# Kernel optimization log

Measured on AMD Instinct MI355X. Metric: run time of the kernel, lower is better.

The kernel has to match this reference:

```python
import jax, jax.numpy as jnp
import numpy as np

N = 50000
E = 800000
DIM_IN, DIM_H, DIM_OUT, HEADS = 128, 8, 32, 15
NEG_SLOPE = 0.2  # PyG GATv2Conv default


def gatv2_layer(x, src, dst, Wl, Wr, att, bias, num_nodes):
    """PyG GATv2Conv (share_weights=False, concat=True) with self-loops already in src/dst.
    x: [N, F_in]; Wl/Wr: [F_in, H*C]; att: [H, C]; bias: [H*C].
    """
    H, C = att.shape
    xl = (x @ Wl).reshape(-1, H, C)  # source transform [N,H,C]
    xr = (x @ Wr).reshape(-1, H, C)  # target transform [N,H,C]
    s = jax.nn.leaky_relu(xl[src] + xr[dst], negative_slope=NEG_SLOPE)  # [E,H,C]
    e = jnp.einsum('ehc,hc->eh', s, att)  # attention logits [E,H]
    # numerically-stable segment softmax over incoming edges of each dst node
    emax = jax.ops.segment_max(e, dst, num_segments=num_nodes)  # [N,H]
    ee = jnp.exp(e - emax[dst])
    denom = jax.ops.segment_sum(ee, dst, num_segments=num_nodes)  # [N,H]
    alpha = ee / denom[dst]  # self-loops guarantee denom > 0
    out = jax.ops.segment_sum(alpha[:, :, None] * xl[src], dst, num_segments=num_nodes)  # [N,H,C]
    return out.reshape(num_nodes, H * C) + bias


def setup_inputs() -> dict:
    key = jax.random.key(0)
    ks = jax.random.split(key, 10)
    x = jax.random.normal(ks[0], (N, DIM_IN), dtype=jnp.float32)
    edge_index = jax.random.randint(ks[1], (2, E), 0, N, dtype=jnp.int64)
    g1 = 1.0 / np.sqrt(DIM_IN)
    g2 = 1.0 / np.sqrt(DIM_H * HEADS)
    return {
        'x': x,
        'edge_index': edge_index,
        'W1l': jax.random.normal(ks[2], (DIM_IN, HEADS * DIM_H), dtype=jnp.float32) * g1,
        'W1r': jax.random.normal(ks[3], (DIM_IN, HEADS * DIM_H), dtype=jnp.float32) * g1,
        'att1': jax.random.normal(ks[4], (HEADS, DIM_H), dtype=jnp.float32) * (1.0 / np.sqrt(DIM_H)),
        'b1': jnp.zeros((HEADS * DIM_H,), dtype=jnp.float32),
        'W2l': jax.random.normal(ks[5], (HEADS * DIM_H, DIM_OUT), dtype=jnp.float32) * g2,
        'W2r': jax.random.normal(ks[6], (HEADS * DIM_H, DIM_OUT), dtype=jnp.float32) * g2,
        'att2': jax.random.normal(ks[7], (1, DIM_OUT), dtype=jnp.float32) * (1.0 / np.sqrt(DIM_OUT)),
        'b2': jnp.zeros((DIM_OUT,), dtype=jnp.float32),
    }


def reference(x, edge_index, W1l, W1r, att1, b1, W2l, W2r, att2, b2):
    n = x.shape[0]
    loops = jnp.arange(n, dtype=edge_index.dtype)
    src = jnp.concatenate([edge_index[0], loops])  # PyG add_self_loops=True
    dst = jnp.concatenate([edge_index[1], loops])
    h = gatv2_layer(x, src, dst, W1l, W1r, att1, b1, n)  # [N, HEADS*DIM_H]
    h = jax.nn.elu(h)
    # dropout(p=0.3) is identity in eval mode
    h = gatv2_layer(h, src, dst, W2l, W2r, att2, b2, n)  # heads=1 -> [N, DIM_OUT]
    return h, jax.nn.log_softmax(h, axis=1)
```

## Files before the change

kernel.cpp:

```cpp
#include <hip/hip_runtime.h>
#include <math.h>

namespace {
constexpr int NN  = 50000;
constexpr int EE  = 800000;
constexpr int FIN = 128;
constexpr int HC1 = 120;
constexpr int F2  = 32;
constexpr int MT  = NN / 16;
constexpr int CAP = 64;
constexpr int NBIN = 64;
constexpr int BINW = 782;
constexpr int BINCAP = 16384;
constexpr int TILE = 4096;
constexpr int ABLK = (EE + TILE - 1) / TILE;
constexpr int CHUNKW = 12500;
}

typedef __attribute__((ext_vector_type(8))) short bf16x8;
typedef __attribute__((ext_vector_type(4))) float f32x4;

template<int CTRL>
__device__ __forceinline__ float dppf(float x) {
    return __int_as_float(__builtin_amdgcn_mov_dpp(__float_as_int(x), CTRL, 0xF, 0xF, true));
}
__device__ __forceinline__ float quad_sum(float x) {
    x += dppf<0xB1>(x);
    x += dppf<0x4E>(x);
    return x;
}
template<int MASK>
__device__ __forceinline__ float swz_add(float x) {
    return x + __int_as_float(__builtin_amdgcn_ds_swizzle(__float_as_int(x), (MASK << 10) | 0x1F));
}
template<int MASK>
__device__ __forceinline__ float swz_max(float x) {
    return fmaxf(x, __int_as_float(__builtin_amdgcn_ds_swizzle(__float_as_int(x), (MASK << 10) | 0x1F)));
}

__device__ __forceinline__ unsigned short f2bf(float f) {
    unsigned int u = __float_as_uint(f);
    unsigned int r = (u + 0x7fffu + ((u >> 16) & 1u)) >> 16;
    return (unsigned short)r;
}
__device__ __forceinline__ float2 bf2f2(unsigned int u) {
    return make_float2(__uint_as_float(u << 16), __uint_as_float(u & 0xffff0000u));
}

__global__ void prep_init_kernel(const unsigned int* __restrict__ raw,
                                 const float* __restrict__ W1l, const float* __restrict__ W1r,
                                 const float* __restrict__ W2l, const float* __restrict__ W2r,
                                 unsigned short* __restrict__ Bf1, unsigned short* __restrict__ Bf2,
                                 int* __restrict__ cursor, int* __restrict__ flag) {
    int tid = blockIdx.x * blockDim.x + threadIdx.x;
    if (blockIdx.x == 0 && threadIdx.x < 64) {
        int t = threadIdx.x;
        unsigned int hi = raw[2 * t + 1];
        unsigned long long ball = __ballot(hi == 0u);
        if (t == 0) *flag = (ball == ~0ULL) ? 1 : 0;
    }
    if (tid < 4096) {
        int t = tid >> 8, lane = tid & 63;
        int kb = (tid >> 6) & 3;
        int k0 = kb * 32 + (lane >> 4) * 8;
        int n = (t & 7) * 16 + (lane & 15);
        const float* W = (t < 8) ? W1l : W1r;
        #pragma unroll
        for (int j = 0; j < 8; ++j)
            Bf1[(size_t)tid * 8 + j] = (n < HC1) ? f2bf(W[(k0 + j) * HC1 + n]) : (unsigned short)0;
    } else if (tid < 5120) {
        int id = tid - 4096;
        int t = id >> 8, lane = id & 63;
        int kb = (id >> 6) & 3;
        int k0 = kb * 32 + (lane >> 4) * 8;
        int nl = (t & 1) * 16 + (lane & 15);
        const float* W = (t < 2) ? W2l : W2r;
        #pragma unroll
        for (int j = 0; j < 8; ++j) {
            int k = k0 + j;
            Bf2[(size_t)id * 8 + j] = (k < HC1) ? f2bf(W[k * F2 + nl]) : (unsigned short)0;
        }
    } else if (tid >= 8192 && tid < 8192 + NBIN) {
        cursor[tid - 8192] = 0;
    }
}

__global__ void __launch_bounds__(256) binA_kernel(
    const unsigned int* __restrict__ raw, const int* __restrict__ flag,
    int* __restrict__ cursor, unsigned int* __restrict__ binbuf) {
    __shared__ int lcnt[NBIN];
    __shared__ int lbase[NBIN];
    __shared__ int lcnt2[NBIN];
    int tid = threadIdx.x;
    int e0 = blockIdx.x * TILE;
    int is64 = *flag;
    if (tid < NBIN) { lcnt[tid] = 0; lcnt2[tid] = 0; }
    __syncthreads();
    #pragma unroll
    for (int i = 0; i < TILE / 256; ++i) {
        int e = e0 + i * 256 + tid;
        if (e < EE) {
            int d = is64 ? (int)raw[2 * (size_t)(EE + e)] : (int)raw[EE + e];
            atomicAdd(&lcnt[d / BINW], 1);
        }
    }
    __syncthreads();
    if (tid < NBIN) {
        int c = lcnt[tid];
        lbase[tid] = (c > 0) ? atomicAdd(&cursor[tid], c) : 0;
    }
    __syncthreads();
    #pragma unroll
    for (int i = 0; i < TILE / 256; ++i) {
        int e = e0 + i * 256 + tid;
        if (e < EE) {
            unsigned int s = is64 ? raw[2 * (size_t)e] : raw[e];
            unsigned int d = is64 ? raw[2 * (size_t)(EE + e)] : raw[EE + e];
            int bin = (int)d / BINW;
            int pos = lbase[bin] + atomicAdd(&lcnt2[bin], 1);
            if (pos < BINCAP) binbuf[(size_t)bin * BINCAP + pos] = (s << 16) | d;
        }
    }
}

__global__ void __launch_bounds__(1024) binB_kernel(
    const int* __restrict__ cursor, const unsigned int* __restrict__ binbuf,
    int* __restrict__ cnt, unsigned short* __restrict__ bucket) {
    __shared__ int lc[BINW * 4];
    int g = blockIdx.x;
    int tid = threadIdx.x;
    int ng0 = g * BINW;
    for (int i = tid; i < BINW * 4; i += 1024) lc[i] = 0;
    __syncthreads();
    int m = min(cursor[g], BINCAP);
    const unsigned int* bb = binbuf + (size_t)g * BINCAP;
    for (int i = tid; i < m; i += 1024) {
        unsigned int u = bb[i];
        int d = (int)(u & 0xffffu);
        int s = (int)(u >> 16);
        atomicAdd(&lc[(d - ng0) * 4 + s / CHUNKW], 1);
    }
    __syncthreads();
    if (tid < BINW) {
        int c0 = lc[tid * 4], c1 = lc[tid * 4 + 1], c2 = lc[tid * 4 + 2], c3 = lc[tid * 4 + 3];
        lc[tid * 4] = 0;
        lc[tid * 4 + 1] = c0;
        lc[tid * 4 + 2] = c0 + c1;
        lc[tid * 4 + 3] = c0 + c1 + c2;
        int n = ng0 + tid;
        if (n < NN) cnt[n] = min(c0 + c1 + c2 + c3, CAP);
    }
    __syncthreads();
    for (int i = tid; i < m; i += 1024) {
        unsigned int u = bb[i];
        int d = (int)(u & 0xffffu);
        int s = (int)(u >> 16);
        int pos = atomicAdd(&lc[(d - ng0) * 4 + s / CHUNKW], 1);
        if (pos < CAP) bucket[(size_t)d * CAP + pos] = (unsigned short)s;
    }
}

__global__ void __launch_bounds__(256) gemm1_mfma_kernel(
    const float* __restrict__ x, const unsigned short* __restrict__ Bf,
    unsigned short* __restrict__ xlb, unsigned short* __restrict__ xrb) {
    int wave = threadIdx.x >> 6, lane = threadIdx.x & 63;
    int mt = blockIdx.x * 4 + wave;
    if (mt >= MT) return;
    int n0 = mt * 16;
    int lr = lane & 15, kg = lane >> 4;
    const float* xrow = x + (size_t)(n0 + lr) * FIN + kg * 8;
    bf16x8 a[4];
    #pragma unroll
    for (int ko = 0; ko < 4; ++ko) {
        float4 lo = *(const float4*)(xrow + ko * 32);
        float4 hi = *(const float4*)(xrow + ko * 32 + 4);
        union { unsigned int u[4]; bf16x8 v; } cv;
        cv.u[0] = f2bf(lo.x) | ((unsigned int)f2bf(lo.y) << 16);
        cv.u[1] = f2bf(lo.z) | ((unsigned int)f2bf(lo.w) << 16);
        cv.u[2] = f2bf(hi.x) | ((unsigned int)f2bf(hi.y) << 16);
        cv.u[3] = f2bf(hi.z) | ((unsigned int)f2bf(hi.w) << 16);
        a[ko] = cv.v;
    }
    const bf16x8* bp = (const bf16x8*)Bf + lane;
    f32x4 acc[16];
    #pragma unroll
    for (int t = 0; t < 16; ++t) acc[t] = (f32x4){0.f, 0.f, 0.f, 0.f};
    #pragma unroll
    for (int t = 0; t < 16; ++t) {
        bf16x8 b0 = bp[(t * 4 + 0) * 64];
        bf16x8 b1 = bp[(t * 4 + 1) * 64];
        bf16x8 b2 = bp[(t * 4 + 2) * 64];
        bf16x8 b3 = bp[(t * 4 + 3) * 64];
        acc[t] = __builtin_amdgcn_mfma_f32_16x16x32_bf16(a[0], b0, acc[t], 0, 0, 0);
        acc[t] = __builtin_amdgcn_mfma_f32_16x16x32_bf16(a[1], b1, acc[t], 0, 0, 0);
        acc[t] = __builtin_amdgcn_mfma_f32_16x16x32_bf16(a[2], b2, acc[t], 0, 0, 0);
        acc[t] = __builtin_amdgcn_mfma_f32_16x16x32_bf16(a[3], b3, acc[t], 0, 0, 0);
    }
    #pragma unroll
    for (int t = 0; t < 16; ++t) {
        unsigned short* outp = (t < 8) ? xlb : xrb;
        int cg = (t & 7) * 16 + lr;
        if (cg < HC1) {
            #pragma unroll
            for (int r = 0; r < 4; ++r)
                outp[(size_t)(n0 + kg * 4 + r) * HC1 + cg] = f2bf(acc[t][r]);
        }
    }
}

__global__ void __launch_bounds__(256) fused1_kernel(
    const unsigned short* __restrict__ bucket, const int* __restrict__ cnt,
    const unsigned short* __restrict__ xlb, const unsigned short* __restrict__ xrb,
    const float* __restrict__ att, const float* __restrict__ b1,
    unsigned int* __restrict__ hout) {
    __shared__ int s_src[4][64];
    int wave = threadIdx.x >> 6;
    int lane = threadIdx.x & 63;
    int n = blockIdx.x * 4 + wave;
    bool act = lane < 60;
    int c0 = act ? 2 * lane : 0;
    float2 xrv = bf2f2(*(const unsigned int*)(xrb + (size_t)n * HC1 + c0));
    float2 atv = *(const float2*)(att + c0);
    int deg = min(cnt[n], CAP);
    int srcv = (lane < deg) ? (int)bucket[(size_t)n * CAP + lane] : 0;
    s_src[wave][lane] = srcv;
    float s, o0, o1;
    {
        unsigned int ua = *(const unsigned int*)(xlb + (size_t)n * HC1 + c0);
        float2 ra = bf2f2(ua);
        float t0 = ra.x + xrv.x; t0 = fmaxf(t0, 0.2f * t0);
        float t1 = ra.y + xrv.y; t1 = fmaxf(t1, 0.2f * t1);
        float pa = quad_sum(atv.x * t0 + atv.y * t1);
        float ea = __expf(fminf(pa, 60.f));
        s = ea; o0 = ea * ra.x; o1 = ea * ra.y;
    }
    for (int j = 0; j < deg; j += 2) {
        int2 ss = *(const int2*)&s_src[wave][j];
        unsigned int ua = *(const unsigned int*)(xlb + (size_t)ss.x * HC1 + c0);
        unsigned int ub = *(const unsigned int*)(xlb + (size_t)ss.y * HC1 + c0);
        float2 ra = bf2f2(ua);
        float2 rb = bf2f2(ub);
        float t0, t1;
        t0 = ra.x + xrv.x; t0 = fmaxf(t0, 0.2f * t0);
        t1 = ra.y + xrv.y; t1 = fmaxf(t1, 0.2f * t1);
        float pa = atv.x * t0 + atv.y * t1;
        t0 = rb.x + xrv.x; t0 = fmaxf(t0, 0.2f * t0);
        t1 = rb.y + xrv.y; t1 = fmaxf(t1, 0.2f * t1);
        float pb = atv.x * t0 + atv.y * t1;
        pa = quad_sum(pa);
        pb = quad_sum(pb);
        float ea = __expf(fminf(pa, 60.f));
        float eb = (j + 1 < deg) ? __expf(fminf(pb, 60.f)) : 0.f;
        s += ea + eb;
        o0 = fmaf(eb, rb.x, fmaf(ea, ra.x, o0));
        o1 = fmaf(eb, rb.y, fmaf(ea, ra.y, o1));
    }
    unsigned int packed = 0u;
    if (act) {
        float inv = 1.0f / s;
        float2 bv = *(const float2*)(b1 + c0);
        float v0 = o0 * inv + bv.x;
        float v1 = o1 * inv + bv.y;
        v0 = v0 > 0.f ? v0 : __expf(v0) - 1.f;
        v1 = v1 > 0.f ? v1 : __expf(v1) - 1.f;
        packed = (unsigned int)f2bf(v0) | ((unsigned int)f2bf(v1) << 16);
    }
    hout[(size_t)n * 64 + lane] = packed;
}

__global__ void __launch_bounds__(256) gemm2_mfma_kernel(
    const unsigned short* __restrict__ hb, const unsigned short* __restrict__ Bf,
    unsigned short* __restrict__ xl2b, unsigned short* __restrict__ xr2b) {
    int wave = threadIdx.x >> 6, lane = threadIdx.x & 63;
    int mt = blockIdx.x * 4 + wave;
    if (mt >= MT) return;
    int n0 = mt * 16;
    int lr = lane & 15, kg = lane >> 4;
    const unsigned short* ab = hb + (size_t)(n0 + lr) * FIN + kg * 8;
    bf16x8 a0 = *(const bf16x8*)(ab);
    bf16x8 a1 = *(const bf16x8*)(ab + 32);
    bf16x8 a2 = *(const bf16x8*)(ab + 64);
    bf16x8 a3 = *(const bf16x8*)(ab + 96);
    const bf16x8* bp = (const bf16x8*)Bf + lane;
    f32x4 acc[4];
    #pragma unroll
    for (int t = 0; t < 4; ++t) acc[t] = (f32x4){0.f, 0.f, 0.f, 0.f};
    #pragma unroll
    for (int t = 0; t < 4; ++t) {
        bf16x8 b0 = bp[(t * 4 + 0) * 64];
        bf16x8 b1 = bp[(t * 4 + 1) * 64];
        bf16x8 b2 = bp[(t * 4 + 2) * 64];
        bf16x8 b3 = bp[(t * 4 + 3) * 64];
        acc[t] = __builtin_amdgcn_mfma_f32_16x16x32_bf16(a0, b0, acc[t], 0, 0, 0);
        acc[t] = __builtin_amdgcn_mfma_f32_16x16x32_bf16(a1, b1, acc[t], 0, 0, 0);
        acc[t] = __builtin_amdgcn_mfma_f32_16x16x32_bf16(a2, b2, acc[t], 0, 0, 0);
        acc[t] = __builtin_amdgcn_mfma_f32_16x16x32_bf16(a3, b3, acc[t], 0, 0, 0);
    }
    #pragma unroll
    for (int t = 0; t < 4; ++t) {
        unsigned short* outp = (t < 2) ? xl2b : xr2b;
        int cg = (t & 1) * 16 + lr;
        #pragma unroll
        for (int r = 0; r < 4; ++r)
            outp[(size_t)(n0 + kg * 4 + r) * F2 + cg] = f2bf(acc[t][r]);
    }
}

__global__ void __launch_bounds__(256) fused2_kernel(
    const unsigned short* __restrict__ bucket, const int* __restrict__ cnt,
    const unsigned short* __restrict__ xl2b, const unsigned short* __restrict__ xr2b,
    const float* __restrict__ att2, const float* __restrict__ b2,
    float* __restrict__ out) {
    __shared__ int s_src[4][64];
    int wave = threadIdx.x >> 6;
    int lane = threadIdx.x & 63;
    int n = blockIdx.x * 4 + wave;
    int grp = lane >> 4;
    int cl = lane & 15;
    int c0 = 2 * cl;
    float2 xrv = bf2f2(*(const unsigned int*)(xr2b + (size_t)n * F2 + c0));
    float2 atv = *(const float2*)(att2 + c0);
    int deg = min(cnt[n], CAP);
    int srcv = (lane < deg) ? (int)bucket[(size_t)n * CAP + lane] : 0;
    s_src[wave][lane] = srcv;
    float s, o0, o1;
    {
        unsigned int u = *(const unsigned int*)(xl2b + (size_t)n * F2 + c0);
        float2 r = bf2f2(u);
        float t0 = r.x + xrv.x; t0 = fmaxf(t0, 0.2f * t0);
        float t1 = r.y + xrv.y; t1 = fmaxf(t1, 0.2f * t1);
        float p = atv.x * t0 + atv.y * t1;
        p = quad_sum(p);
        p = swz_add<4>(p);
        p = swz_add<8>(p);
        float e = (grp == 0) ? __expf(fminf(p, 60.f)) : 0.f;
        s = e; o0 = e * r.x; o1 = e * r.y;
    }
    for (int j = 0; j < deg; j += 4) {
        int myj = j + grp;
        int src = s_src[wave][min(myj, 63)];
        bool val = myj < deg;
        unsigned int u = *(const unsigned int*)(xl2b + (size_t)src * F2 + c0);
        float2 r = bf2f2(u);
        float t0 = r.x + xrv.x; t0 = fmaxf(t0, 0.2f * t0);
        float t1 = r.y + xrv.y; t1 = fmaxf(t1, 0.2f * t1);
        float p = atv.x * t0 + atv.y * t1;
        p = quad_sum(p);
        p = swz_add<4>(p);
        p = swz_add<8>(p);
        float e = val ? __expf(fminf(p, 60.f)) : 0.f;
        s += e;
        o0 = fmaf(e, r.x, o0);
        o1 = fmaf(e, r.y, o1);
    }
    s  = swz_add<16>(s);   s  += __shfl_xor(s, 32);
    o0 = swz_add<16>(o0);  o0 += __shfl_xor(o0, 32);
    o1 = swz_add<16>(o1);  o1 += __shfl_xor(o1, 32);
    float2 bv = *(const float2*)(b2 + c0);
    float inv = 1.0f / s;
    float v0 = o0 * inv + bv.x;
    float v1 = o1 * inv + bv.y;
    float mm = fmaxf(v0, v1);
    mm = fmaxf(mm, dppf<0xB1>(mm));
    mm = fmaxf(mm, dppf<0x4E>(mm));
    mm = swz_max<4>(mm);
    mm = swz_max<8>(mm);
    float se = __expf(v0 - mm) + __expf(v1 - mm);
    se += dppf<0xB1>(se);
    se += dppf<0x4E>(se);
    se = swz_add<4>(se);
    se = swz_add<8>(se);
    float lse = mm + __logf(se);
    if (lane < 16) {
        *(float2*)(out + (size_t)n * F2 + c0) = make_float2(v0, v1);
        *(float2*)(out + (size_t)NN * F2 + (size_t)n * F2 + c0) =
            make_float2(v0 - lse, v1 - lse);
    }
}

extern "C" void kernel_launch(void* const* d_in, const int* in_sizes, int n_in,
                              void* d_out, int out_size, void* d_ws, size_t ws_size,
                              hipStream_t stream) {
    const float* x    = (const float*)d_in[0];
    const unsigned int* ei_raw = (const unsigned int*)d_in[1];
    const float* W1l  = (const float*)d_in[2];
    const float* W1r  = (const float*)d_in[3];
    const float* att1 = (const float*)d_in[4];
    const float* b1   = (const float*)d_in[5];
    const float* W2l  = (const float*)d_in[6];
    const float* W2r  = (const float*)d_in[7];
    const float* att2 = (const float*)d_in[8];
    const float* b2   = (const float*)d_in[9];
    float* out = (float*)d_out;

    char* ws = (char*)d_ws;
    unsigned short* XR1b = (unsigned short*)ws; ws += (size_t)NN * HC1 * 2;
    unsigned int* HHb    = (unsigned int*)ws;   ws += (size_t)NN * 64 * 4;
    unsigned short* XR2b = (unsigned short*)ws; ws += (size_t)NN * F2 * 2;
    unsigned short* XL1b = (unsigned short*)ws; ws += (size_t)NN * HC1 * 2;
    unsigned short* XL2b = (unsigned short*)ws; ws += (size_t)NN * F2 * 2;
    unsigned short* BF1  = (unsigned short*)ws; ws += 16 * 4 * 64 * 8 * 2;
    unsigned short* BF2  = (unsigned short*)ws; ws += 4 * 4 * 64 * 8 * 2;
    unsigned short* BUCKET = (unsigned short*)ws; ws += (size_t)NN * CAP * 2;
    unsigned int* BINBUF = (unsigned int*)ws;   ws += (size_t)NBIN * BINCAP * 4;
    int* CURSOR = (int*)ws;                     ws += NBIN * 4;
    int* CNT    = (int*)ws;                     ws += (size_t)NN * 4;
    int* FLAG   = (int*)ws;

    prep_init_kernel<<<64, 256, 0, stream>>>(ei_raw, W1l, W1r, W2l, W2r,
                                             BF1, BF2, CURSOR, FLAG);

    binA_kernel<<<ABLK, 256, 0, stream>>>(ei_raw, FLAG, CURSOR, BINBUF);
    binB_kernel<<<NBIN, 1024, 0, stream>>>(CURSOR, BINBUF, CNT, BUCKET);

    gemm1_mfma_kernel<<<(MT + 3) / 4, 256, 0, stream>>>(x, BF1, XL1b, XR1b);
    fused1_kernel<<<NN / 4, 256, 0, stream>>>(BUCKET, CNT, XL1b, XR1b, att1, b1, HHb);

    gemm2_mfma_kernel<<<(MT + 3) / 4, 256, 0, stream>>>(
        (const unsigned short*)HHb, BF2, XL2b, XR2b);
    fused2_kernel<<<NN / 4, 256, 0, stream>>>(BUCKET, CNT, XL2b, XR2b, att2, b2, out);
}
```

Measured before the change: 214.0 us.

## Merge prep into binning kernel, pad feature rows to 128, use exp2

Folds the weight-conversion prep and the int64-detection flag into the binning kernel, so one launch does both and the cursor is cleared with a memset. The layer-1 bf16 feature buffers are padded from 120 to 128 columns, giving aligned row strides and shift-based indexing and removing the store guard in the GEMM. Attention weights are pre-scaled by log2(e) so exp2f replaces __expf, and the clamp is raised to keep the same range. Padding increases the memory footprint and gather bandwidth slightly, and the merged kernel mixes two different workloads in one grid.

```diff
diff --git a/kernel.cpp b/kernel.cpp
--- a/kernel.cpp
+++ b/kernel.cpp
@@ -6,6 +6,7 @@
 constexpr int EE  = 800000;
 constexpr int FIN = 128;
 constexpr int HC1 = 120;
+constexpr int PAD = 128;
 constexpr int F2  = 32;
 constexpr int MT  = NN / 16;
 constexpr int CAP = 64;
@@ -15,6 +16,8 @@
 constexpr int TILE = 4096;
 constexpr int ABLK = (EE + TILE - 1) / TILE;
 constexpr int CHUNKW = 12500;
+constexpr int GB = (MT + 3) / 4;
+constexpr float LOG2E = 1.442695041f;
 }
 
 typedef __attribute__((ext_vector_type(8))) short bf16x8;
@@ -47,18 +50,54 @@
     return make_float2(__uint_as_float(u << 16), __uint_as_float(u & 0xffff0000u));
 }
 
-__global__ void prep_init_kernel(const unsigned int* __restrict__ raw,
-                                 const float* __restrict__ W1l, const float* __restrict__ W1r,
-                                 const float* __restrict__ W2l, const float* __restrict__ W2r,
-                                 unsigned short* __restrict__ Bf1, unsigned short* __restrict__ Bf2,
-                                 int* __restrict__ cursor, int* __restrict__ flag) {
-    int tid = blockIdx.x * blockDim.x + threadIdx.x;
-    if (blockIdx.x == 0 && threadIdx.x < 64) {
-        int t = threadIdx.x;
-        unsigned int hi = raw[2 * t + 1];
+
+__device__ void binA_body(int b, const unsigned int* __restrict__ raw,
+                          int* __restrict__ cursor, unsigned int* __restrict__ binbuf) {
+    __shared__ int lcnt[NBIN];
+    __shared__ int lbase[NBIN];
+    __shared__ int lcnt2[NBIN];
+    __shared__ int is64_s;
+    int tid = threadIdx.x;
+    if (tid < NBIN) { lcnt[tid] = 0; lcnt2[tid] = 0; }
+    if (tid < 64) {
+        unsigned int hi = raw[2 * tid + 1];
         unsigned long long ball = __ballot(hi == 0u);
-        if (t == 0) *flag = (ball == ~0ULL) ? 1 : 0;
-    }
+        if (tid == 0) is64_s = (ball == ~0ULL) ? 1 : 0;
+    }
+    __syncthreads();
+    int is64 = is64_s;
+    int e0 = b * TILE;
+    #pragma unroll
+    for (int i = 0; i < TILE / 256; ++i) {
+        int e = e0 + i * 256 + tid;
+        if (e < EE) {
+            int d = is64 ? (int)raw[2 * (size_t)(EE + e)] : (int)raw[EE + e];
+            atomicAdd(&lcnt[d / BINW], 1);
+        }
+    }
+    __syncthreads();
+    if (tid < NBIN) {
+        int c = lcnt[tid];
+        lbase[tid] = (c > 0) ? atomicAdd(&cursor[tid], c) : 0;
+    }
+    __syncthreads();
+    #pragma unroll
+    for (int i = 0; i < TILE / 256; ++i) {
+        int e = e0 + i * 256 + tid;
+        if (e < EE) {
+            unsigned int s = is64 ? raw[2 * (size_t)e] : raw[e];
+            unsigned int d = is64 ? raw[2 * (size_t)(EE + e)] : raw[EE + e];
+            int bin = (int)d / BINW;
+            int pos = lbase[bin] + atomicAdd(&lcnt2[bin], 1);
+            if (pos < BINCAP) binbuf[(size_t)bin * BINCAP + pos] = (s << 16) | d;
+        }
+    }
+}
+
+__device__ void prep_body(int p, const float* __restrict__ W1l, const float* __restrict__ W1r,
+                          const float* __restrict__ W2l, const float* __restrict__ W2r,
+                          unsigned short* __restrict__ Bf1, unsigned short* __restrict__ Bf2) {
+    int tid = p * 256 + threadIdx.x;
     if (tid < 4096) {
         int t = tid >> 8, lane = tid & 63;
         int kb = (tid >> 6) & 3;
@@ -68,7 +107,7 @@
         #pragma unroll
         for (int j = 0; j < 8; ++j)
             Bf1[(size_t)tid * 8 + j] = (n < HC1) ? f2bf(W[(k0 + j) * HC1 + n]) : (unsigned short)0;
-    } else if (tid < 5120) {
+    } else {
         int id = tid - 4096;
         int t = id >> 8, lane = id & 63;
         int kb = (id >> 6) & 3;
@@ -80,47 +119,17 @@
             int k = k0 + j;
             Bf2[(size_t)id * 8 + j] = (k < HC1) ? f2bf(W[k * F2 + nl]) : (unsigned short)0;
         }
-    } else if (tid >= 8192 && tid < 8192 + NBIN) {
-        cursor[tid - 8192] = 0;
-    }
-}
-
-__global__ void __launch_bounds__(256) binA_kernel(
-    const unsigned int* __restrict__ raw, const int* __restrict__ flag,
-    int* __restrict__ cursor, unsigned int* __restrict__ binbuf) {
-    __shared__ int lcnt[NBIN];
-    __shared__ int lbase[NBIN];
-    __shared__ int lcnt2[NBIN];
-    int tid = threadIdx.x;
-    int e0 = blockIdx.x * TILE;
-    int is64 = *flag;
-    if (tid < NBIN) { lcnt[tid] = 0; lcnt2[tid] = 0; }
-    __syncthreads();
-    #pragma unroll
-    for (int i = 0; i < TILE / 256; ++i) {
-        int e = e0 + i * 256 + tid;
-        if (e < EE) {
-            int d = is64 ? (int)raw[2 * (size_t)(EE + e)] : (int)raw[EE + e];
-            atomicAdd(&lcnt[d / BINW], 1);
-        }
-    }
-    __syncthreads();
-    if (tid < NBIN) {
-        int c = lcnt[tid];
-        lbase[tid] = (c > 0) ? atomicAdd(&cursor[tid], c) : 0;
-    }
-    __syncthreads();
-    #pragma unroll
-    for (int i = 0; i < TILE / 256; ++i) {
-        int e = e0 + i * 256 + tid;
-        if (e < EE) {
-            unsigned int s = is64 ? raw[2 * (size_t)e] : raw[e];
-            unsigned int d = is64 ? raw[2 * (size_t)(EE + e)] : raw[EE + e];
-            int bin = (int)d / BINW;
-            int pos = lbase[bin] + atomicAdd(&lcnt2[bin], 1);
-            if (pos < BINCAP) binbuf[(size_t)bin * BINCAP + pos] = (s << 16) | d;
-        }
-    }
+    }
+}
+
+__global__ void __launch_bounds__(256) mergeA_kernel(
+    const unsigned int* __restrict__ raw, int* __restrict__ cursor,
+    unsigned int* __restrict__ binbuf,
+    const float* __restrict__ W1l, const float* __restrict__ W1r,
+    const float* __restrict__ W2l, const float* __restrict__ W2r,
+    unsigned short* __restrict__ Bf1, unsigned short* __restrict__ Bf2) {
+    if (blockIdx.x < ABLK) binA_body(blockIdx.x, raw, cursor, binbuf);
+    else                   prep_body(blockIdx.x - ABLK, W1l, W1r, W2l, W2r, Bf1, Bf2);
 }
 
 __global__ void __launch_bounds__(1024) binB_kernel(
@@ -200,11 +209,9 @@
     for (int t = 0; t < 16; ++t) {
         unsigned short* outp = (t < 8) ? xlb : xrb;
         int cg = (t & 7) * 16 + lr;
-        if (cg < HC1) {
-            #pragma unroll
-            for (int r = 0; r < 4; ++r)
-                outp[(size_t)(n0 + kg * 4 + r) * HC1 + cg] = f2bf(acc[t][r]);
-        }
+        #pragma unroll
+        for (int r = 0; r < 4; ++r)
+            outp[((size_t)(n0 + kg * 4 + r) << 7) + cg] = f2bf(acc[t][r]);
     }
 }
 
@@ -219,25 +226,26 @@
     int n = blockIdx.x * 4 + wave;
     bool act = lane < 60;
     int c0 = act ? 2 * lane : 0;
-    float2 xrv = bf2f2(*(const unsigned int*)(xrb + (size_t)n * HC1 + c0));
+    float2 xrv = bf2f2(*(const unsigned int*)(xrb + ((size_t)n << 7) + c0));
     float2 atv = *(const float2*)(att + c0);
+    atv.x *= LOG2E; atv.y *= LOG2E;
     int deg = min(cnt[n], CAP);
     int srcv = (lane < deg) ? (int)bucket[(size_t)n * CAP + lane] : 0;
     s_src[wave][lane] = srcv;
     float s, o0, o1;
     {
-        unsigned int ua = *(const unsigned int*)(xlb + (size_t)n * HC1 + c0);
+        unsigned int ua = *(const unsigned int*)(xlb + ((size_t)n << 7) + c0);
         float2 ra = bf2f2(ua);
         float t0 = ra.x + xrv.x; t0 = fmaxf(t0, 0.2f * t0);
         float t1 = ra.y + xrv.y; t1 = fmaxf(t1, 0.2f * t1);
         float pa = quad_sum(atv.x * t0 + atv.y * t1);
-        float ea = __expf(fminf(pa, 60.f));
+        float ea = exp2f(fminf(pa, 86.f));
         s = ea; o0 = ea * ra.x; o1 = ea * ra.y;
     }
     for (int j = 0; j < deg; j += 2) {
         int2 ss = *(const int2*)&s_src[wave][j];
-        unsigned int ua = *(const unsigned int*)(xlb + (size_t)ss.x * HC1 + c0);
-        unsigned int ub = *(const unsigned int*)(xlb + (size_t)ss.y * HC1 + c0);
+        unsigned int ua = *(const unsigned int*)(xlb + ((size_t)ss.x << 7) + c0);
+        unsigned int ub = *(const unsigned int*)(xlb + ((size_t)ss.y << 7) + c0);
         float2 ra = bf2f2(ua);
         float2 rb = bf2f2(ub);
         float t0, t1;
@@ -249,8 +257,8 @@
         float pb = atv.x * t0 + atv.y * t1;
         pa = quad_sum(pa);
         pb = quad_sum(pb);
-        float ea = __expf(fminf(pa, 60.f));
-        float eb = (j + 1 < deg) ? __expf(fminf(pb, 60.f)) : 0.f;
+        float ea = exp2f(fminf(pa, 86.f));
+        float eb = (j + 1 < deg) ? exp2f(fminf(pb, 86.f)) : 0.f;
         s += ea + eb;
         o0 = fmaf(eb, rb.x, fmaf(ea, ra.x, o0));
         o1 = fmaf(eb, rb.y, fmaf(ea, ra.y, o1));
@@ -320,6 +328,7 @@
     int c0 = 2 * cl;
     float2 xrv = bf2f2(*(const unsigned int*)(xr2b + (size_t)n * F2 + c0));
     float2 atv = *(const float2*)(att2 + c0);
+    atv.x *= LOG2E; atv.y *= LOG2E;
     int deg = min(cnt[n], CAP);
     int srcv = (lane < deg) ? (int)bucket[(size_t)n * CAP + lane] : 0;
     s_src[wave][lane] = srcv;
@@ -333,7 +342,7 @@
         p = quad_sum(p);
         p = swz_add<4>(p);
         p = swz_add<8>(p);
-        float e = (grp == 0) ? __expf(fminf(p, 60.f)) : 0.f;
+        float e = (grp == 0) ? exp2f(fminf(p, 86.f)) : 0.f;
         s = e; o0 = e * r.x; o1 = e * r.y;
     }
     for (int j = 0; j < deg; j += 4) {
@@ -348,7 +357,7 @@
         p = quad_sum(p);
         p = swz_add<4>(p);
         p = swz_add<8>(p);
-        float e = val ? __expf(fminf(p, 60.f)) : 0.f;
+        float e = val ? exp2f(fminf(p, 86.f)) : 0.f;
         s += e;
         o0 = fmaf(e, r.x, o0);
         o1 = fmaf(e, r.y, o1);
@@ -394,29 +403,24 @@
     float* out = (float*)d_out;
 
     char* ws = (char*)d_ws;
-    unsigned short* XR1b = (unsigned short*)ws; ws += (size_t)NN * HC1 * 2;
+    unsigned short* XL1b = (unsigned short*)ws; ws += (size_t)NN * PAD * 2;
+    unsigned short* XR1b = (unsigned short*)ws; ws += (size_t)NN * PAD * 2;
     unsigned int* HHb    = (unsigned int*)ws;   ws += (size_t)NN * 64 * 4;
+    unsigned short* XL2b = (unsigned short*)ws; ws += (size_t)NN * F2 * 2;
     unsigned short* XR2b = (unsigned short*)ws; ws += (size_t)NN * F2 * 2;
-    unsigned short* XL1b = (unsigned short*)ws; ws += (size_t)NN * HC1 * 2;
-    unsigned short* XL2b = (unsigned short*)ws; ws += (size_t)NN * F2 * 2;
     unsigned short* BF1  = (unsigned short*)ws; ws += 16 * 4 * 64 * 8 * 2;
     unsigned short* BF2  = (unsigned short*)ws; ws += 4 * 4 * 64 * 8 * 2;
     unsigned short* BUCKET = (unsigned short*)ws; ws += (size_t)NN * CAP * 2;
     unsigned int* BINBUF = (unsigned int*)ws;   ws += (size_t)NBIN * BINCAP * 4;
     int* CURSOR = (int*)ws;                     ws += NBIN * 4;
     int* CNT    = (int*)ws;                     ws += (size_t)NN * 4;
-    int* FLAG   = (int*)ws;
-
-    prep_init_kernel<<<64, 256, 0, stream>>>(ei_raw, W1l, W1r, W2l, W2r,
-                                             BF1, BF2, CURSOR, FLAG);
-
-    binA_kernel<<<ABLK, 256, 0, stream>>>(ei_raw, FLAG, CURSOR, BINBUF);
+
+    hipMemsetAsync(CURSOR, 0, NBIN * sizeof(int), stream);
+    mergeA_kernel<<<ABLK + 20, 256, 0, stream>>>(ei_raw, CURSOR, BINBUF,
+                                                 W1l, W1r, W2l, W2r, BF1, BF2);
     binB_kernel<<<NBIN, 1024, 0, stream>>>(CURSOR, BINBUF, CNT, BUCKET);
-
-    gemm1_mfma_kernel<<<(MT + 3) / 4, 256, 0, stream>>>(x, BF1, XL1b, XR1b);
+    gemm1_mfma_kernel<<<GB, 256, 0, stream>>>(x, BF1, XL1b, XR1b);
     fused1_kernel<<<NN / 4, 256, 0, stream>>>(BUCKET, CNT, XL1b, XR1b, att1, b1, HHb);
-
-    gemm2_mfma_kernel<<<(MT + 3) / 4, 256, 0, stream>>>(
-        (const unsigned short*)HHb, BF2, XL2b, XR2b);
+    gemm2_mfma_kernel<<<GB, 256, 0, stream>>>((const unsigned short*)HHb, BF2, XL2b, XR2b);
     fused2_kernel<<<NN / 4, 256, 0, stream>>>(BUCKET, CNT, XL2b, XR2b, att2, b2, out);
 }
```

New measurement: 213.9 us. About the same (-0.1%).
